# Kernel tuning notes

Measured on AMD Instinct MI355X. Metric: run time of the kernel, lower is better.

## Reference

```python
import jax, jax.numpy as jnp
import numpy as np

N = 100000   # nodes
E = 1600000  # edges (avg degree 16)
D = 128      # in_feats
H = 128      # n_hidden
C = 64       # n_classes


def setup_inputs() -> dict:
    key = jax.random.key(0)
    ks = jax.random.split(key, 9)
    x = jax.random.normal(ks[0], (N, D), dtype=jnp.float32)
    src = jax.random.randint(ks[1], (E,), 0, N, dtype=jnp.int32)
    dst = jax.random.randint(ks[2], (E,), 0, N, dtype=jnp.int32)
    s = 1.0 / np.sqrt(D)
    W1 = jax.random.uniform(ks[3], (H, D), jnp.float32, -s, s)
    b1 = jax.random.uniform(ks[4], (H,), jnp.float32, -s, s)
    sh = 1.0 / np.sqrt(H)
    W2 = jax.random.uniform(ks[5], (H, H), jnp.float32, -sh, sh)
    b2 = jax.random.uniform(ks[6], (H,), jnp.float32, -sh, sh)
    W3 = jax.random.uniform(ks[7], (C, H), jnp.float32, -sh, sh)
    b3 = jax.random.uniform(ks[8], (C,), jnp.float32, -sh, sh)
    return {"x": x, "src": src, "dst": dst,
            "W1": W1, "b1": b1, "W2": W2, "b2": b2, "W3": W3, "b3": b3}


def reference(x, src, dst, W1, b1, W2, b2, W3, b3):
    n = x.shape[0]
    # in-degrees of destination nodes (DGL g.in_degrees())
    deg = jax.ops.segment_sum(jnp.ones_like(dst, dtype=x.dtype), dst, num_segments=n)
    norm = 1.0 / (deg + 1.0)  # [N]

    def sage_gcn(h, W, b, act):
        # gather src features, sum into dst (copy_u + sum reduce)
        m = jax.ops.segment_sum(h[src], dst, num_segments=n)  # [N, d]
        h_neigh = (m + h) * norm[:, None]                      # include self, /(deg+1)
        o = h_neigh @ W.T + b                                  # fc_neigh
        return jax.nn.relu(o) if act else o

    h = sage_gcn(x, W1, b1, True)
    h = sage_gcn(h, W2, b2, True)   # dropout is identity in eval mode
    return sage_gcn(h, W3, b3, False)
```

## Files before the change

### kernel.cpp

```cpp
#include <hip/hip_runtime.h>
#include <hip/hip_fp16.h>

typedef _Float16 f16x8 __attribute__((ext_vector_type(8)));
typedef _Float16 f16x4 __attribute__((ext_vector_type(4)));
typedef float    f32x4 __attribute__((ext_vector_type(4)));


#define PSHIFT 6
#define PNODES 64
#define BMAX   2048
#define NBLK   64

__global__ __launch_bounds__(512) void k_hist(const int* __restrict__ dst, int E, int chunk,
                                              int B, int* __restrict__ histT) {
    __shared__ int hist[BMAX];
    int blk = blockIdx.x, t = threadIdx.x;
    for (int k = t; k < B; k += 512) hist[k] = 0;
    __syncthreads();
    int lo = blk * chunk, hi = min(lo + chunk, E);
    for (int i = lo + t; i < hi; i += 512) atomicAdd(&hist[dst[i] >> PSHIFT], 1);
    __syncthreads();
    for (int k = t; k < B; k += 512) histT[k * NBLK + blk] = hist[k];
}

__global__ __launch_bounds__(256) void k_scanA(const int* __restrict__ histT, int total,
                                               int* __restrict__ psum) {
    __shared__ int sd[256];
    int t = threadIdx.x;
    int base = blockIdx.x * 1024 + t * 4;
    int s = 0;
    if (base + 3 < total) {
        int4 v = *(const int4*)(histT + base);
        s = v.x + v.y + v.z + v.w;
    } else {
        for (int j = 0; j < 4; j++) if (base + j < total) s += histT[base + j];
    }
    sd[t] = s;
    __syncthreads();
    for (int off = 128; off > 0; off >>= 1) {
        if (t < off) sd[t] += sd[t + off];
        __syncthreads();
    }
    if (t == 0) psum[blockIdx.x] = sd[0];
}

__global__ __launch_bounds__(128) void k_scanB(const int* __restrict__ psum, int G,
                                               int* __restrict__ pbase,
                                               int* __restrict__ bbase, int B,
                                               int* __restrict__ offsets, int n, int E) {
    __shared__ int sd[128];
    int t = threadIdx.x;
    int v = (t < G) ? psum[t] : 0;
    sd[t] = v;
    __syncthreads();
    int acc = v;
    for (int off = 1; off < 128; off <<= 1) {
        int u = (t >= off) ? sd[t - off] : 0;
        __syncthreads();
        acc += u;
        sd[t] = acc;
        __syncthreads();
    }
    if (t < G) pbase[t] = acc - v;
    if (t == 0) { bbase[B] = E; offsets[n] = E; }
}

__global__ __launch_bounds__(256) void k_scanC(int* __restrict__ histT, int total,
                                               const int* __restrict__ pbase,
                                               int* __restrict__ bbase) {
    __shared__ int sd[256];
    int t = threadIdx.x;
    int base = blockIdx.x * 1024 + t * 4;
    int v[4];
    int s = 0;
    bool full = (base + 3 < total);
    if (full) {
        int4 q = *(const int4*)(histT + base);
        v[0] = q.x; v[1] = q.y; v[2] = q.z; v[3] = q.w;
        s = q.x + q.y + q.z + q.w;
    } else {
#pragma unroll
        for (int j = 0; j < 4; j++) { v[j] = (base + j < total) ? histT[base + j] : 0; s += v[j]; }
    }
    sd[t] = s;
    __syncthreads();
    int acc = s;
    for (int off = 1; off < 256; off <<= 1) {
        int u = (t >= off) ? sd[t - off] : 0;
        __syncthreads();
        acc += u;
        sd[t] = acc;
        __syncthreads();
    }
    int run = pbase[blockIdx.x] + (acc - s);
    int o[4];
#pragma unroll
    for (int j = 0; j < 4; j++) { o[j] = run; run += v[j]; }
    if (full) *(int4*)(histT + base) = make_int4(o[0], o[1], o[2], o[3]);
    else { for (int j = 0; j < 4; j++) if (base + j < total) histT[base + j] = o[j]; }
    if ((base & 63) == 0 && base < total) bbase[base >> 6] = o[0];
}

__global__ __launch_bounds__(512) void k_place(const int* __restrict__ src,
                                               const int* __restrict__ dst,
                                               const int* __restrict__ histT,
                                               int E, int chunk, int B,
                                               unsigned int* __restrict__ ebuf) {
    __shared__ int cur[BMAX];
    int blk = blockIdx.x, t = threadIdx.x;
    for (int k = t; k < B; k += 512) cur[k] = histT[k * NBLK + blk];
    __syncthreads();
    int lo = blk * chunk, hi = min(lo + chunk, E);
    for (int i = lo + t; i < hi; i += 512) {
        int d = dst[i], s = src[i];
        int k = d >> PSHIFT;
        int pos = atomicAdd(&cur[k], 1);
        ebuf[pos] = ((unsigned)(d & (PNODES - 1)) << 17) | (unsigned)s;
    }
}

__global__ __launch_bounds__(256) void k_binB(const unsigned int* __restrict__ ebuf,
                                              const int* __restrict__ bbase,
                                              int* __restrict__ offsets,
                                              float* __restrict__ norm,
                                              int* __restrict__ cols, int n) {
    __shared__ int hist[PNODES];
    __shared__ int lofs[PNODES];
    __shared__ int cur[PNODES];
    int b = blockIdx.x;
    int t = threadIdx.x;
    int base = bbase[b];
    int cnt = bbase[b + 1] - base;
    const unsigned int* bd = ebuf + base;

    if (t < PNODES) hist[t] = 0;
    __syncthreads();
    for (int e = t; e < cnt; e += 256) atomicAdd(&hist[bd[e] >> 17], 1);
    __syncthreads();
    if (t < PNODES) lofs[t] = hist[t];
    __syncthreads();
    for (int off = 1; off < PNODES; off <<= 1) {
        int v = 0;
        if (t < PNODES && t >= off) v = lofs[t - off];
        __syncthreads();
        if (t < PNODES) lofs[t] += v;
        __syncthreads();
    }
    if (t < PNODES) {
        int excl = lofs[t] - hist[t];
        cur[t] = excl;
        int node = (b << PSHIFT) + t;
        if (node < n) {
            offsets[node] = base + excl;
            norm[node] = 1.0f / ((float)hist[t] + 1.0f);
        }
    }
    __syncthreads();
    for (int e = t; e < cnt; e += 256) {
        unsigned v = bd[e];
        int local = v >> 17;
        int s = (int)(v & 0x1FFFF);
        int r = atomicAdd(&cur[local], 1);
        cols[base + r] = s;
    }
}


template <int KOUT, bool IN_F32>
__global__ __launch_bounds__(256) void k_gemm_mfma(const void* __restrict__ Ain,
                                                   const float* __restrict__ W,
                                                   _Float16* __restrict__ outh, int n) {
    constexpr int NT = KOUT / 16;
    __shared__ _Float16 A_lds[128 * 136];
    __shared__ _Float16 W_lds[KOUT * 136];

    int tid  = threadIdx.x;
    int lane = tid & 63;
    int wave = tid >> 6;
    int m0   = blockIdx.x * 128;

    for (int i = tid; i < KOUT * 16; i += 256) {
        int r = i >> 4, c = i & 15;
        float4 u0 = *(const float4*)(W + (size_t)r * 128 + c * 8);
        float4 u1 = *(const float4*)(W + (size_t)r * 128 + c * 8 + 4);
        f16x8 v;
        v[0] = (_Float16)u0.x; v[1] = (_Float16)u0.y;
        v[2] = (_Float16)u0.z; v[3] = (_Float16)u0.w;
        v[4] = (_Float16)u1.x; v[5] = (_Float16)u1.y;
        v[6] = (_Float16)u1.z; v[7] = (_Float16)u1.w;
        *(f16x8*)&W_lds[r * 136 + c * 8] = v;
    }
    if constexpr (IN_F32) {
        const float* A = (const float*)Ain;
        for (int i = tid; i < 2048; i += 256) {
            int r = i >> 4, c = i & 15;
            int gm = m0 + r;
            f16x8 v = {};
            if (gm < n) {
                float4 u0 = *(const float4*)(A + (size_t)gm * 128 + c * 8);
                float4 u1 = *(const float4*)(A + (size_t)gm * 128 + c * 8 + 4);
                v[0] = (_Float16)u0.x; v[1] = (_Float16)u0.y;
                v[2] = (_Float16)u0.z; v[3] = (_Float16)u0.w;
                v[4] = (_Float16)u1.x; v[5] = (_Float16)u1.y;
                v[6] = (_Float16)u1.z; v[7] = (_Float16)u1.w;
            }
            *(f16x8*)&A_lds[r * 136 + c * 8] = v;
        }
    } else {
        const _Float16* A = (const _Float16*)Ain;
        for (int i = tid; i < 2048; i += 256) {
            int r = i >> 4, c = i & 15;
            int gm = m0 + r;
            f16x8 v = {};
            if (gm < n) v = ((const f16x8*)(A + (size_t)gm * 128))[c];
            *(f16x8*)&A_lds[r * 136 + c * 8] = v;
        }
    }
    __syncthreads();

    int m0w = wave * 32;
    int lr  = lane & 15;
    int lk  = (lane >> 4) * 4;

    f32x4 acc[2][NT];
#pragma unroll
    for (int mi = 0; mi < 2; mi++)
#pragma unroll
        for (int ni = 0; ni < NT; ni++) acc[mi][ni] = (f32x4){0.f, 0.f, 0.f, 0.f};

#pragma unroll
    for (int kk = 0; kk < 8; kk++) {
        int k0 = kk * 16;
        f16x4 a0 = *(const f16x4*)&A_lds[(m0w + lr) * 136 + k0 + lk];
        f16x4 a1 = *(const f16x4*)&A_lds[(m0w + 16 + lr) * 136 + k0 + lk];
#pragma unroll
        for (int ni = 0; ni < NT; ni++) {
            f16x4 b = *(const f16x4*)&W_lds[(ni * 16 + lr) * 136 + k0 + lk];
            acc[0][ni] = __builtin_amdgcn_mfma_f32_16x16x16f16(a0, b, acc[0][ni], 0, 0, 0);
            acc[1][ni] = __builtin_amdgcn_mfma_f32_16x16x16f16(a1, b, acc[1][ni], 0, 0, 0);
        }
    }

    int orow = (lane >> 4) * 4;
#pragma unroll
    for (int mi = 0; mi < 2; mi++) {
#pragma unroll
        for (int r = 0; r < 4; r++) {
            int gm = m0 + m0w + mi * 16 + orow + r;
            if (gm < n) {
                _Float16* op = outh + (size_t)gm * KOUT + lr;
#pragma unroll
                for (int ni = 0; ni < NT; ni++)
                    op[ni * 16] = (_Float16)acc[mi][ni][r];
            }
        }
    }
}


__global__ __launch_bounds__(256) void k_agg128_br(const _Float16* __restrict__ g,
                                                   const int* __restrict__ offs,
                                                   const int* __restrict__ cols,
                                                   const float* __restrict__ norm,
                                                   const float* __restrict__ bias,
                                                   _Float16* __restrict__ hout, int n) {
    int node = blockIdx.x * 16 + (threadIdx.x >> 4);
    if (node >= n) return;
    int lane = threadIdx.x & 15;

    f16x8 sv = ((const f16x8*)(g + (size_t)node * 128))[lane];
    float acc[8];
#pragma unroll
    for (int j = 0; j < 8; j++) acc[j] = (float)sv[j];

    int p = offs[node], e = offs[node + 1];
    for (; p + 8 <= e; p += 8) {
        int c0 = cols[p],     c1 = cols[p + 1], c2 = cols[p + 2], c3 = cols[p + 3];
        int c4 = cols[p + 4], c5 = cols[p + 5], c6 = cols[p + 6], c7 = cols[p + 7];
        f16x8 a0 = ((const f16x8*)(g + (size_t)c0 * 128))[lane];
        f16x8 a1 = ((const f16x8*)(g + (size_t)c1 * 128))[lane];
        f16x8 a2 = ((const f16x8*)(g + (size_t)c2 * 128))[lane];
        f16x8 a3 = ((const f16x8*)(g + (size_t)c3 * 128))[lane];
        f16x8 a4 = ((const f16x8*)(g + (size_t)c4 * 128))[lane];
        f16x8 a5 = ((const f16x8*)(g + (size_t)c5 * 128))[lane];
        f16x8 a6 = ((const f16x8*)(g + (size_t)c6 * 128))[lane];
        f16x8 a7 = ((const f16x8*)(g + (size_t)c7 * 128))[lane];
#pragma unroll
        for (int j = 0; j < 8; j++)
            acc[j] += (((float)a0[j] + (float)a1[j]) + ((float)a2[j] + (float)a3[j]))
                    + (((float)a4[j] + (float)a5[j]) + ((float)a6[j] + (float)a7[j]));
    }
    for (; p + 4 <= e; p += 4) {
        int c0 = cols[p], c1 = cols[p + 1], c2 = cols[p + 2], c3 = cols[p + 3];
        f16x8 a0 = ((const f16x8*)(g + (size_t)c0 * 128))[lane];
        f16x8 a1 = ((const f16x8*)(g + (size_t)c1 * 128))[lane];
        f16x8 a2 = ((const f16x8*)(g + (size_t)c2 * 128))[lane];
        f16x8 a3 = ((const f16x8*)(g + (size_t)c3 * 128))[lane];
#pragma unroll
        for (int j = 0; j < 8; j++)
            acc[j] += ((float)a0[j] + (float)a1[j]) + ((float)a2[j] + (float)a3[j]);
    }
    for (; p < e; p++) {
        f16x8 a = ((const f16x8*)(g + (size_t)cols[p] * 128))[lane];
#pragma unroll
        for (int j = 0; j < 8; j++) acc[j] += (float)a[j];
    }
    float nm = norm[node];
    float4 bb0 = ((const float4*)bias)[lane * 2];
    float4 bb1 = ((const float4*)bias)[lane * 2 + 1];
    float o[8];
    o[0] = acc[0] * nm + bb0.x; o[1] = acc[1] * nm + bb0.y;
    o[2] = acc[2] * nm + bb0.z; o[3] = acc[3] * nm + bb0.w;
    o[4] = acc[4] * nm + bb1.x; o[5] = acc[5] * nm + bb1.y;
    o[6] = acc[6] * nm + bb1.z; o[7] = acc[7] * nm + bb1.w;
    f16x8 ov;
#pragma unroll
    for (int j = 0; j < 8; j++) ov[j] = (_Float16)fmaxf(o[j], 0.f);
    ((f16x8*)(hout + (size_t)node * 128))[lane] = ov;
}

__global__ __launch_bounds__(256) void k_agg64_b(const _Float16* __restrict__ g,
                                                 const int* __restrict__ offs,
                                                 const int* __restrict__ cols,
                                                 const float* __restrict__ norm,
                                                 const float* __restrict__ bias,
                                                 float* __restrict__ out, int n) {
    int node = blockIdx.x * 16 + (threadIdx.x >> 4);
    if (node >= n) return;
    int lane = threadIdx.x & 15;

    f16x4 sv = ((const f16x4*)(g + (size_t)node * 64))[lane];
    float acc[4];
#pragma unroll
    for (int j = 0; j < 4; j++) acc[j] = (float)sv[j];

    int p = offs[node], e = offs[node + 1];
    for (; p + 8 <= e; p += 8) {
        int c0 = cols[p],     c1 = cols[p + 1], c2 = cols[p + 2], c3 = cols[p + 3];
        int c4 = cols[p + 4], c5 = cols[p + 5], c6 = cols[p + 6], c7 = cols[p + 7];
        f16x4 a0 = ((const f16x4*)(g + (size_t)c0 * 64))[lane];
        f16x4 a1 = ((const f16x4*)(g + (size_t)c1 * 64))[lane];
        f16x4 a2 = ((const f16x4*)(g + (size_t)c2 * 64))[lane];
        f16x4 a3 = ((const f16x4*)(g + (size_t)c3 * 64))[lane];
        f16x4 a4 = ((const f16x4*)(g + (size_t)c4 * 64))[lane];
        f16x4 a5 = ((const f16x4*)(g + (size_t)c5 * 64))[lane];
        f16x4 a6 = ((const f16x4*)(g + (size_t)c6 * 64))[lane];
        f16x4 a7 = ((const f16x4*)(g + (size_t)c7 * 64))[lane];
#pragma unroll
        for (int j = 0; j < 4; j++)
            acc[j] += (((float)a0[j] + (float)a1[j]) + ((float)a2[j] + (float)a3[j]))
                    + (((float)a4[j] + (float)a5[j]) + ((float)a6[j] + (float)a7[j]));
    }
    for (; p + 4 <= e; p += 4) {
        int c0 = cols[p], c1 = cols[p + 1], c2 = cols[p + 2], c3 = cols[p + 3];
        f16x4 a0 = ((const f16x4*)(g + (size_t)c0 * 64))[lane];
        f16x4 a1 = ((const f16x4*)(g + (size_t)c1 * 64))[lane];
        f16x4 a2 = ((const f16x4*)(g + (size_t)c2 * 64))[lane];
        f16x4 a3 = ((const f16x4*)(g + (size_t)c3 * 64))[lane];
#pragma unroll
        for (int j = 0; j < 4; j++)
            acc[j] += ((float)a0[j] + (float)a1[j]) + ((float)a2[j] + (float)a3[j]);
    }
    for (; p < e; p++) {
        f16x4 a = ((const f16x4*)(g + (size_t)cols[p] * 64))[lane];
#pragma unroll
        for (int j = 0; j < 4; j++) acc[j] += (float)a[j];
    }
    float nm = norm[node];
    float4 bb = ((const float4*)bias)[lane];
    float* op = out + (size_t)node * 64 + lane * 4;
    *(float4*)op = make_float4(acc[0] * nm + bb.x, acc[1] * nm + bb.y,
                               acc[2] * nm + bb.z, acc[3] * nm + bb.w);
}


extern "C" void kernel_launch(void* const* d_in, const int* in_sizes, int n_in,
                              void* d_out, int out_size, void* d_ws, size_t ws_size,
                              hipStream_t stream) {
    const float* x  = (const float*)d_in[0];
    const int*  src = (const int*)d_in[1];
    const int*  dst = (const int*)d_in[2];
    const float* W1 = (const float*)d_in[3];
    const float* b1 = (const float*)d_in[4];
    const float* W2 = (const float*)d_in[5];
    const float* b2 = (const float*)d_in[6];
    const float* W3 = (const float*)d_in[7];
    const float* b3 = (const float*)d_in[8];
    float* out = (float*)d_out;

    int n = in_sizes[0] / 128;
    int E = in_sizes[1];
    int B = (n + PNODES - 1) >> PSHIFT;
    int total = B * NBLK;
    int chunk = (E + NBLK - 1) / NBLK;
    int G1 = (total + 1023) / 1024;

    char* ws = (char*)d_ws;
    size_t off = 0;
    auto alloc = [&](size_t bytes) -> char* {
        char* p = ws + off;
        off += (bytes + 255) & ~(size_t)255;
        return p;
    };
    int*      bbase   = (int*)alloc(((size_t)B + 1) * 4);
    int*      offsets = (int*)alloc(((size_t)n + 1) * 4);
    float*    norm    = (float*)alloc((size_t)n * 4);
    int*      psum    = (int*)alloc(256 * 4);
    int*      pbase   = (int*)alloc(256 * 4);
    int*      cols    = (int*)alloc((size_t)E * 4);
    _Float16* bufA    = (_Float16*)alloc((size_t)n * 128 * 2);
    _Float16* bufB    = (_Float16*)alloc((size_t)n * 128 * 2);

    unsigned int* ebuf  = (unsigned int*)bufA;
    int*          histT = (int*)((char*)bufA + (size_t)8 * 1024 * 1024);

    k_hist <<<NBLK, 512, 0, stream>>>(dst, E, chunk, B, histT);
    k_scanA<<<G1, 256, 0, stream>>>(histT, total, psum);
    k_scanB<<<1, 128, 0, stream>>>(psum, G1, pbase, bbase, B, offsets, n, E);
    k_scanC<<<G1, 256, 0, stream>>>(histT, total, pbase, bbase);
    k_place<<<NBLK, 512, 0, stream>>>(src, dst, histT, E, chunk, B, ebuf);
    k_binB <<<B, 256, 0, stream>>>(ebuf, bbase, offsets, norm, cols, n);

    int nblkG = (n + 127) / 128;
    int nblkA = (n + 15) / 16;

    k_gemm_mfma<128, true><<<nblkG, 256, 0, stream>>>(x, W1, bufA, n);
    k_agg128_br<<<nblkA, 256, 0, stream>>>(bufA, offsets, cols, norm, b1, bufB, n);
    k_gemm_mfma<128, false><<<nblkG, 256, 0, stream>>>(bufB, W2, bufA, n);
    k_agg128_br<<<nblkA, 256, 0, stream>>>(bufA, offsets, cols, norm, b2, bufB, n);
    k_gemm_mfma<64, false><<<nblkG, 256, 0, stream>>>(bufB, W3, bufA, n);
    k_agg64_b<<<nblkA, 256, 0, stream>>>(bufA, offsets, cols, norm, b3, out, n);
}
```

Baseline: 280.3 us.

## Fuse neighbor aggregation into following GEMM and double CSR-build block count

Merges each 128-wide aggregation (gather-sum, normalize, bias, ReLU) with the next layer's MFMA GEMM. Aggregated rows go straight into LDS instead of a global buffer, which removes two kernel launches and an intermediate write and read. It also doubles the number of histogram/placement blocks used to build the CSR (scan widened to match) and drops the 8-way unrolled gather loops. The risk is that the fused kernel runs one block per 128 nodes with large LDS. That lowers occupancy and the parallelism available to hide gather latency, compared with the former 16-nodes-per-block aggregation.

```diff
diff --git a/kernel.cpp b/kernel.cpp
--- a/kernel.cpp
+++ b/kernel.cpp
@@ -9,7 +9,7 @@
 #define PSHIFT 6
 #define PNODES 64
 #define BMAX   2048
-#define NBLK   64
+#define NBLK   128
 
 __global__ __launch_bounds__(512) void k_hist(const int* __restrict__ dst, int E, int chunk,
                                               int B, int* __restrict__ histT) {
@@ -44,17 +44,17 @@
     if (t == 0) psum[blockIdx.x] = sd[0];
 }
 
-__global__ __launch_bounds__(128) void k_scanB(const int* __restrict__ psum, int G,
+__global__ __launch_bounds__(256) void k_scanB(const int* __restrict__ psum, int G,
                                                int* __restrict__ pbase,
                                                int* __restrict__ bbase, int B,
                                                int* __restrict__ offsets, int n, int E) {
-    __shared__ int sd[128];
+    __shared__ int sd[256];
     int t = threadIdx.x;
     int v = (t < G) ? psum[t] : 0;
     sd[t] = v;
     __syncthreads();
     int acc = v;
-    for (int off = 1; off < 128; off <<= 1) {
+    for (int off = 1; off < 256; off <<= 1) {
         int u = (t >= off) ? sd[t - off] : 0;
         __syncthreads();
         acc += u;
@@ -98,7 +98,7 @@
     for (int j = 0; j < 4; j++) { o[j] = run; run += v[j]; }
     if (full) *(int4*)(histT + base) = make_int4(o[0], o[1], o[2], o[3]);
     else { for (int j = 0; j < 4; j++) if (base + j < total) histT[base + j] = o[j]; }
-    if ((base & 63) == 0 && base < total) bbase[base >> 6] = o[0];
+    if ((base & (NBLK - 1)) == 0 && base < total) bbase[base / NBLK] = o[0];
 }
 
 __global__ __launch_bounds__(512) void k_place(const int* __restrict__ src,
@@ -166,20 +166,18 @@
 }
 
 
-template <int KOUT, bool IN_F32>
-__global__ __launch_bounds__(256) void k_gemm_mfma(const void* __restrict__ Ain,
-                                                   const float* __restrict__ W,
-                                                   _Float16* __restrict__ outh, int n) {
-    constexpr int NT = KOUT / 16;
+__global__ __launch_bounds__(256) void k_gemm_mfma_f32in(const float* __restrict__ A,
+                                                         const float* __restrict__ W,
+                                                         _Float16* __restrict__ outh, int n) {
     __shared__ _Float16 A_lds[128 * 136];
-    __shared__ _Float16 W_lds[KOUT * 136];
+    __shared__ _Float16 W_lds[128 * 136];
 
     int tid  = threadIdx.x;
     int lane = tid & 63;
     int wave = tid >> 6;
     int m0   = blockIdx.x * 128;
 
-    for (int i = tid; i < KOUT * 16; i += 256) {
+    for (int i = tid; i < 128 * 16; i += 256) {
         int r = i >> 4, c = i & 15;
         float4 u0 = *(const float4*)(W + (size_t)r * 128 + c * 8);
         float4 u1 = *(const float4*)(W + (size_t)r * 128 + c * 8 + 4);
@@ -190,134 +188,191 @@
         v[6] = (_Float16)u1.z; v[7] = (_Float16)u1.w;
         *(f16x8*)&W_lds[r * 136 + c * 8] = v;
     }
-    if constexpr (IN_F32) {
-        const float* A = (const float*)Ain;
-        for (int i = tid; i < 2048; i += 256) {
-            int r = i >> 4, c = i & 15;
-            int gm = m0 + r;
-            f16x8 v = {};
+    for (int i = tid; i < 2048; i += 256) {
+        int r = i >> 4, c = i & 15;
+        int gm = m0 + r;
+        f16x8 v = {};
+        if (gm < n) {
+            float4 u0 = *(const float4*)(A + (size_t)gm * 128 + c * 8);
+            float4 u1 = *(const float4*)(A + (size_t)gm * 128 + c * 8 + 4);
+            v[0] = (_Float16)u0.x; v[1] = (_Float16)u0.y;
+            v[2] = (_Float16)u0.z; v[3] = (_Float16)u0.w;
+            v[4] = (_Float16)u1.x; v[5] = (_Float16)u1.y;
+            v[6] = (_Float16)u1.z; v[7] = (_Float16)u1.w;
+        }
+        *(f16x8*)&A_lds[r * 136 + c * 8] = v;
+    }
+    __syncthreads();
+
+    int m0w = wave * 32;
+    int lr  = lane & 15;
+    int lk  = (lane >> 4) * 4;
+
+    f32x4 acc[2][8];
+#pragma unroll
+    for (int mi = 0; mi < 2; mi++)
+#pragma unroll
+        for (int ni = 0; ni < 8; ni++) acc[mi][ni] = (f32x4){0.f, 0.f, 0.f, 0.f};
+
+#pragma unroll
+    for (int kk = 0; kk < 8; kk++) {
+        int k0 = kk * 16;
+        f16x4 a0 = *(const f16x4*)&A_lds[(m0w + lr) * 136 + k0 + lk];
+        f16x4 a1 = *(const f16x4*)&A_lds[(m0w + 16 + lr) * 136 + k0 + lk];
+#pragma unroll
+        for (int ni = 0; ni < 8; ni++) {
+            f16x4 b = *(const f16x4*)&W_lds[(ni * 16 + lr) * 136 + k0 + lk];
+            acc[0][ni] = __builtin_amdgcn_mfma_f32_16x16x16f16(a0, b, acc[0][ni], 0, 0, 0);
+            acc[1][ni] = __builtin_amdgcn_mfma_f32_16x16x16f16(a1, b, acc[1][ni], 0, 0, 0);
+        }
+    }
+
+    int orow = (lane >> 4) * 4;
+#pragma unroll
+    for (int mi = 0; mi < 2; mi++) {
+#pragma unroll
+        for (int r = 0; r < 4; r++) {
+            int gm = m0 + m0w + mi * 16 + orow + r;
             if (gm < n) {
-                float4 u0 = *(const float4*)(A + (size_t)gm * 128 + c * 8);
-                float4 u1 = *(const float4*)(A + (size_t)gm * 128 + c * 8 + 4);
+                _Float16* op = outh + (size_t)gm * 128 + lr;
+#pragma unroll
+                for (int ni = 0; ni < 8; ni++)
+                    op[ni * 16] = (_Float16)acc[mi][ni][r];
+            }
+        }
+    }
+}
+
+
+template <int KOUT>
+__global__ __launch_bounds__(256) void k_agg_gemm(const _Float16* __restrict__ g,
+                                                  const int* __restrict__ offs,
+                                                  const int* __restrict__ cols,
+                                                  const float* __restrict__ norm,
+                                                  const float* __restrict__ bias,
+                                                  const float* __restrict__ W,
+                                                  _Float16* __restrict__ outg, int n) {
+    __shared__ _Float16 A_lds[128 * 136];
+    __shared__ _Float16 W_lds[64 * 136];
+
+    int tid  = threadIdx.x;
+    int lane = tid & 63;
+    int wave = tid >> 6;
+    int m0   = blockIdx.x * 128;
+    int l16  = tid & 15;
+    int n16  = tid >> 4;
+
+    for (int i = tid; i < 64 * 16; i += 256) {
+        int r = i >> 4, c = i & 15;
+        float4 u0 = *(const float4*)(W + (size_t)r * 128 + c * 8);
+        float4 u1 = *(const float4*)(W + (size_t)r * 128 + c * 8 + 4);
+        f16x8 v;
+        v[0] = (_Float16)u0.x; v[1] = (_Float16)u0.y;
+        v[2] = (_Float16)u0.z; v[3] = (_Float16)u0.w;
+        v[4] = (_Float16)u1.x; v[5] = (_Float16)u1.y;
+        v[6] = (_Float16)u1.z; v[7] = (_Float16)u1.w;
+        *(f16x8*)&W_lds[r * 136 + c * 8] = v;
+    }
+
+    for (int sub = 0; sub < 8; sub++) {
+        int row  = sub * 16 + n16;
+        int node = m0 + row;
+        f16x8 hv = {};
+        if (node < n) {
+            f16x8 sv = ((const f16x8*)(g + (size_t)node * 128))[l16];
+            float acc[8];
+#pragma unroll
+            for (int j = 0; j < 8; j++) acc[j] = (float)sv[j];
+
+            int p = offs[node], e = offs[node + 1];
+            for (; p + 4 <= e; p += 4) {
+                int c0 = cols[p], c1 = cols[p + 1], c2 = cols[p + 2], c3 = cols[p + 3];
+                f16x8 a0 = ((const f16x8*)(g + (size_t)c0 * 128))[l16];
+                f16x8 a1 = ((const f16x8*)(g + (size_t)c1 * 128))[l16];
+                f16x8 a2 = ((const f16x8*)(g + (size_t)c2 * 128))[l16];
+                f16x8 a3 = ((const f16x8*)(g + (size_t)c3 * 128))[l16];
+#pragma unroll
+                for (int j = 0; j < 8; j++)
+                    acc[j] += ((float)a0[j] + (float)a1[j]) + ((float)a2[j] + (float)a3[j]);
+            }
+            for (; p < e; p++) {
+                f16x8 a = ((const f16x8*)(g + (size_t)cols[p] * 128))[l16];
+#pragma unroll
+                for (int j = 0; j < 8; j++) acc[j] += (float)a[j];
+            }
+            float nm = norm[node];
+            float4 bb0 = ((const float4*)bias)[l16 * 2];
+            float4 bb1 = ((const float4*)bias)[l16 * 2 + 1];
+            float o[8];
+            o[0] = acc[0] * nm + bb0.x; o[1] = acc[1] * nm + bb0.y;
+            o[2] = acc[2] * nm + bb0.z; o[3] = acc[3] * nm + bb0.w;
+            o[4] = acc[4] * nm + bb1.x; o[5] = acc[5] * nm + bb1.y;
+            o[6] = acc[6] * nm + bb1.z; o[7] = acc[7] * nm + bb1.w;
+#pragma unroll
+            for (int j = 0; j < 8; j++) hv[j] = (_Float16)fmaxf(o[j], 0.f);
+        }
+        *(f16x8*)&A_lds[row * 136 + l16 * 8] = hv;
+    }
+    __syncthreads();
+
+    int m0w = wave * 32;
+    int lr  = lane & 15;
+    int lk  = (lane >> 4) * 4;
+    int orow = (lane >> 4) * 4;
+
+#pragma unroll
+    for (int hf = 0; hf < KOUT / 64; hf++) {
+        if (hf > 0) {
+            __syncthreads();
+            for (int i = tid; i < 64 * 16; i += 256) {
+                int r = i >> 4, c = i & 15;
+                float4 u0 = *(const float4*)(W + (size_t)(hf * 64 + r) * 128 + c * 8);
+                float4 u1 = *(const float4*)(W + (size_t)(hf * 64 + r) * 128 + c * 8 + 4);
+                f16x8 v;
                 v[0] = (_Float16)u0.x; v[1] = (_Float16)u0.y;
                 v[2] = (_Float16)u0.z; v[3] = (_Float16)u0.w;
                 v[4] = (_Float16)u1.x; v[5] = (_Float16)u1.y;
                 v[6] = (_Float16)u1.z; v[7] = (_Float16)u1.w;
-            }
-            *(f16x8*)&A_lds[r * 136 + c * 8] = v;
-        }
-    } else {
-        const _Float16* A = (const _Float16*)Ain;
-        for (int i = tid; i < 2048; i += 256) {
-            int r = i >> 4, c = i & 15;
-            int gm = m0 + r;
-            f16x8 v = {};
-            if (gm < n) v = ((const f16x8*)(A + (size_t)gm * 128))[c];
-            *(f16x8*)&A_lds[r * 136 + c * 8] = v;
-        }
-    }
-    __syncthreads();
-
-    int m0w = wave * 32;
-    int lr  = lane & 15;
-    int lk  = (lane >> 4) * 4;
-
-    f32x4 acc[2][NT];
-#pragma unroll
-    for (int mi = 0; mi < 2; mi++)
-#pragma unroll
-        for (int ni = 0; ni < NT; ni++) acc[mi][ni] = (f32x4){0.f, 0.f, 0.f, 0.f};
-
-#pragma unroll
-    for (int kk = 0; kk < 8; kk++) {
-        int k0 = kk * 16;
-        f16x4 a0 = *(const f16x4*)&A_lds[(m0w + lr) * 136 + k0 + lk];
-        f16x4 a1 = *(const f16x4*)&A_lds[(m0w + 16 + lr) * 136 + k0 + lk];
-#pragma unroll
-        for (int ni = 0; ni < NT; ni++) {
-            f16x4 b = *(const f16x4*)&W_lds[(ni * 16 + lr) * 136 + k0 + lk];
-            acc[0][ni] = __builtin_amdgcn_mfma_f32_16x16x16f16(a0, b, acc[0][ni], 0, 0, 0);
-            acc[1][ni] = __builtin_amdgcn_mfma_f32_16x16x16f16(a1, b, acc[1][ni], 0, 0, 0);
-        }
-    }
-
-    int orow = (lane >> 4) * 4;
-#pragma unroll
-    for (int mi = 0; mi < 2; mi++) {
-#pragma unroll
-        for (int r = 0; r < 4; r++) {
-            int gm = m0 + m0w + mi * 16 + orow + r;
-            if (gm < n) {
-                _Float16* op = outh + (size_t)gm * KOUT + lr;
-#pragma unroll
-                for (int ni = 0; ni < NT; ni++)
-                    op[ni * 16] = (_Float16)acc[mi][ni][r];
-            }
-        }
-    }
-}
-
-
-__global__ __launch_bounds__(256) void k_agg128_br(const _Float16* __restrict__ g,
-                                                   const int* __restrict__ offs,
-                                                   const int* __restrict__ cols,
-                                                   const float* __restrict__ norm,
-                                                   const float* __restrict__ bias,
-                                                   _Float16* __restrict__ hout, int n) {
-    int node = blockIdx.x * 16 + (threadIdx.x >> 4);
-    if (node >= n) return;
-    int lane = threadIdx.x & 15;
-
-    f16x8 sv = ((const f16x8*)(g + (size_t)node * 128))[lane];
-    float acc[8];
-#pragma unroll
-    for (int j = 0; j < 8; j++) acc[j] = (float)sv[j];
-
-    int p = offs[node], e = offs[node + 1];
-    for (; p + 8 <= e; p += 8) {
-        int c0 = cols[p],     c1 = cols[p + 1], c2 = cols[p + 2], c3 = cols[p + 3];
-        int c4 = cols[p + 4], c5 = cols[p + 5], c6 = cols[p + 6], c7 = cols[p + 7];
-        f16x8 a0 = ((const f16x8*)(g + (size_t)c0 * 128))[lane];
-        f16x8 a1 = ((const f16x8*)(g + (size_t)c1 * 128))[lane];
-        f16x8 a2 = ((const f16x8*)(g + (size_t)c2 * 128))[lane];
-        f16x8 a3 = ((const f16x8*)(g + (size_t)c3 * 128))[lane];
-        f16x8 a4 = ((const f16x8*)(g + (size_t)c4 * 128))[lane];
-        f16x8 a5 = ((const f16x8*)(g + (size_t)c5 * 128))[lane];
-        f16x8 a6 = ((const f16x8*)(g + (size_t)c6 * 128))[lane];
-        f16x8 a7 = ((const f16x8*)(g + (size_t)c7 * 128))[lane];
-#pragma unroll
-        for (int j = 0; j < 8; j++)
-            acc[j] += (((float)a0[j] + (float)a1[j]) + ((float)a2[j] + (float)a3[j]))
-                    + (((float)a4[j] + (float)a5[j]) + ((float)a6[j] + (float)a7[j]));
-    }
-    for (; p + 4 <= e; p += 4) {
-        int c0 = cols[p], c1 = cols[p + 1], c2 = cols[p + 2], c3 = cols[p + 3];
-        f16x8 a0 = ((const f16x8*)(g + (size_t)c0 * 128))[lane];
-        f16x8 a1 = ((const f16x8*)(g + (size_t)c1 * 128))[lane];
-        f16x8 a2 = ((const f16x8*)(g + (size_t)c2 * 128))[lane];
-        f16x8 a3 = ((const f16x8*)(g + (size_t)c3 * 128))[lane];
-#pragma unroll
-        for (int j = 0; j < 8; j++)
-            acc[j] += ((float)a0[j] + (float)a1[j]) + ((float)a2[j] + (float)a3[j]);
-    }
-    for (; p < e; p++) {
-        f16x8 a = ((const f16x8*)(g + (size_t)cols[p] * 128))[lane];
-#pragma unroll
-        for (int j = 0; j < 8; j++) acc[j] += (float)a[j];
-    }
-    float nm = norm[node];
-    float4 bb0 = ((const float4*)bias)[lane * 2];
-    float4 bb1 = ((const float4*)bias)[lane * 2 + 1];
-    float o[8];
-    o[0] = acc[0] * nm + bb0.x; o[1] = acc[1] * nm + bb0.y;
-    o[2] = acc[2] * nm + bb0.z; o[3] = acc[3] * nm + bb0.w;
-    o[4] = acc[4] * nm + bb1.x; o[5] = acc[5] * nm + bb1.y;
-    o[6] = acc[6] * nm + bb1.z; o[7] = acc[7] * nm + bb1.w;
-    f16x8 ov;
-#pragma unroll
-    for (int j = 0; j < 8; j++) ov[j] = (_Float16)fmaxf(o[j], 0.f);
-    ((f16x8*)(hout + (size_t)node * 128))[lane] = ov;
-}
+                *(f16x8*)&W_lds[r * 136 + c * 8] = v;
+            }
+            __syncthreads();
+        }
+
+        f32x4 acc[2][4];
+#pragma unroll
+        for (int mi = 0; mi < 2; mi++)
+#pragma unroll
+            for (int ni = 0; ni < 4; ni++) acc[mi][ni] = (f32x4){0.f, 0.f, 0.f, 0.f};
+
+#pragma unroll
+        for (int kk = 0; kk < 8; kk++) {
+            int k0 = kk * 16;
+            f16x4 a0 = *(const f16x4*)&A_lds[(m0w + lr) * 136 + k0 + lk];
+            f16x4 a1 = *(const f16x4*)&A_lds[(m0w + 16 + lr) * 136 + k0 + lk];
+#pragma unroll
+            for (int ni = 0; ni < 4; ni++) {
+                f16x4 b = *(const f16x4*)&W_lds[(ni * 16 + lr) * 136 + k0 + lk];
+                acc[0][ni] = __builtin_amdgcn_mfma_f32_16x16x16f16(a0, b, acc[0][ni], 0, 0, 0);
+                acc[1][ni] = __builtin_amdgcn_mfma_f32_16x16x16f16(a1, b, acc[1][ni], 0, 0, 0);
+            }
+        }
+
+#pragma unroll
+        for (int mi = 0; mi < 2; mi++) {
+#pragma unroll
+            for (int r = 0; r < 4; r++) {
+                int gm = m0 + m0w + mi * 16 + orow + r;
+                if (gm < n) {
+                    _Float16* op = outg + (size_t)gm * KOUT + hf * 64 + lr;
+#pragma unroll
+                    for (int ni = 0; ni < 4; ni++)
+                        op[ni * 16] = (_Float16)acc[mi][ni][r];
+                }
+            }
+        }
+    }
+}
+
 
 __global__ __launch_bounds__(256) void k_agg64_b(const _Float16* __restrict__ g,
                                                  const int* __restrict__ offs,
@@ -335,22 +390,6 @@
     for (int j = 0; j < 4; j++) acc[j] = (float)sv[j];
 
     int p = offs[node], e = offs[node + 1];
-    for (; p + 8 <= e; p += 8) {
-        int c0 = cols[p],     c1 = cols[p + 1], c2 = cols[p + 2], c3 = cols[p + 3];
-        int c4 = cols[p + 4], c5 = cols[p + 5], c6 = cols[p + 6], c7 = cols[p + 7];
-        f16x4 a0 = ((const f16x4*)(g + (size_t)c0 * 64))[lane];
-        f16x4 a1 = ((const f16x4*)(g + (size_t)c1 * 64))[lane];
-        f16x4 a2 = ((const f16x4*)(g + (size_t)c2 * 64))[lane];
-        f16x4 a3 = ((const f16x4*)(g + (size_t)c3 * 64))[lane];
-        f16x4 a4 = ((const f16x4*)(g + (size_t)c4 * 64))[lane];
-        f16x4 a5 = ((const f16x4*)(g + (size_t)c5 * 64))[lane];
-        f16x4 a6 = ((const f16x4*)(g + (size_t)c6 * 64))[lane];
-        f16x4 a7 = ((const f16x4*)(g + (size_t)c7 * 64))[lane];
-#pragma unroll
-        for (int j = 0; j < 4; j++)
-            acc[j] += (((float)a0[j] + (float)a1[j]) + ((float)a2[j] + (float)a3[j]))
-                    + (((float)a4[j] + (float)a5[j]) + ((float)a6[j] + (float)a7[j]));
-    }
     for (; p + 4 <= e; p += 4) {
         int c0 = cols[p], c1 = cols[p + 1], c2 = cols[p + 2], c3 = cols[p + 3];
         f16x4 a0 = ((const f16x4*)(g + (size_t)c0 * 64))[lane];
@@ -416,7 +455,7 @@
 
     k_hist <<<NBLK, 512, 0, stream>>>(dst, E, chunk, B, histT);
     k_scanA<<<G1, 256, 0, stream>>>(histT, total, psum);
-    k_scanB<<<1, 128, 0, stream>>>(psum, G1, pbase, bbase, B, offsets, n, E);
+    k_scanB<<<1, 256, 0, stream>>>(psum, G1, pbase, bbase, B, offsets, n, E);
     k_scanC<<<G1, 256, 0, stream>>>(histT, total, pbase, bbase);
     k_place<<<NBLK, 512, 0, stream>>>(src, dst, histT, E, chunk, B, ebuf);
     k_binB <<<B, 256, 0, stream>>>(ebuf, bbase, offsets, norm, cols, n);
@@ -424,10 +463,8 @@
     int nblkG = (n + 127) / 128;
     int nblkA = (n + 15) / 16;
 
-    k_gemm_mfma<128, true><<<nblkG, 256, 0, stream>>>(x, W1, bufA, n);
-    k_agg128_br<<<nblkA, 256, 0, stream>>>(bufA, offsets, cols, norm, b1, bufB, n);
-    k_gemm_mfma<128, false><<<nblkG, 256, 0, stream>>>(bufB, W2, bufA, n);
-    k_agg128_br<<<nblkA, 256, 0, stream>>>(bufA, offsets, cols, norm, b2, bufB, n);
-    k_gemm_mfma<64, false><<<nblkG, 256, 0, stream>>>(bufB, W3, bufA, n);
+    k_gemm_mfma_f32in<<<nblkG, 256, 0, stream>>>(x, W1, bufA, n);
+    k_agg_gemm<128><<<nblkG, 256, 0, stream>>>(bufA, offsets, cols, norm, b1, W2, bufB, n);
+    k_agg_gemm<64><<<nblkG, 256, 0, stream>>>(bufB, offsets, cols, norm, b2, W3, bufA, n);
     k_agg64_b<<<nblkA, 256, 0, stream>>>(bufA, offsets, cols, norm, b3, out, n);
 }
```

After: 331.9 us. 1.18x slower.
